# Kernel tuning notes

Measured on AMD Instinct MI355X. Metric: run time of the kernel, lower is better.

The kernel has to match this reference:

```python
import jax, jax.numpy as jnp
import numpy as np
import math

N, IN, H = 50000, 64, 128      # nodes, input feat, hidden dim
SH, HD = 8, 16                 # structural heads, dim per head (SH*HD == H)
TH, THD = 4, 32                # temporal heads, head dim
T, E, C = 8, 400000, 10        # snapshots, edges per snapshot, classes


def _ln(x, g, b):
    mu = jnp.mean(x, -1, keepdims=True)
    var = jnp.mean((x - mu) ** 2, -1, keepdims=True)
    return (x - mu) * jax.lax.rsqrt(var + 1e-5) * g + b


def _gat(x, ei, Wg, a, g, b):
    # x: [N,H], ei: [2,E]. Multi-head GAT with scatter softmax over dst.
    n = x.shape[0]
    h = (x @ Wg.T).reshape(n, SH, HD)
    src, dst = ei[0], ei[1]
    hs = h[src]                                  # [E,SH,HD] gathered src feats
    hd_ = h[dst]                                 # [E,SH,HD]
    s = jnp.concatenate([hs, hd_], -1) @ a       # [E,SH] shared attn vector per head
    s = jnp.where(s > 0, s, 0.2 * s)             # LeakyReLU(0.2)
    m = jax.ops.segment_max(s, dst, num_segments=n)   # [N,SH]
    e = jnp.exp(s - m[dst])
    z = jax.ops.segment_sum(e, dst, num_segments=n)   # [N,SH]
    alpha = e / z[dst]                           # scatter softmax per dst node
    msg = hs * alpha[..., None]                  # [E,SH,HD]
    out = jax.ops.segment_sum(msg.reshape(-1, SH * HD), dst, num_segments=n)
    out = out + x                                # residual (Identity: in_dim == SH*HD)
    return jax.nn.elu(_ln(out, g, b))


def setup_inputs():
    key = jax.random.key(0)
    ks = jax.random.split(key, 10)
    def xu(k, shape):
        lim = math.sqrt(6.0 / (shape[0] + shape[-1]))
        return jax.random.uniform(k, shape, minval=-lim, maxval=lim, dtype=jnp.float32)
    return {
        'x_original': jax.random.normal(ks[0], (N, IN), dtype=jnp.float32),
        'edge_indices': jax.random.randint(ks[1], (T, 2, E), 0, N),
        'node_masks': jnp.ones((T, N), dtype=jnp.int32),
        'Wp': xu(ks[2], (H, IN)), 'bp': jnp.zeros(H),
        'Wg': xu(ks[3], (H, H)),
        'a_attn': xu(ks[4], (1, 2 * HD))[0],
        'ln1_g': jnp.ones(H), 'ln1_b': jnp.zeros(H),
        'Wqkv': xu(ks[5], (3 * H, H)), 'bqkv': jnp.zeros(3 * H),
        'Wo': xu(ks[6], (H, H)), 'bo': jnp.zeros(H),
        'ln2_g': jnp.ones(H), 'ln2_b': jnp.zeros(H),
        'Wc': xu(ks[7], (C, H)), 'bc': jnp.zeros(C),
    }


def reference(x_original, edge_indices, node_masks, Wp, bp, Wg, a_attn, ln1_g, ln1_b,
              Wqkv, bqkv, Wo, bo, ln2_g, ln2_b, Wc, bc):
    # input projection (dropout is identity in eval)
    x = jax.nn.elu(x_original @ Wp.T + bp)                      # [N,H]
    # structural attention per snapshot (scan keeps one snapshot's edge buffers live)
    def step(_, ei):
        return None, _gat(x, ei, Wg, a_attn, ln1_g, ln1_b)
    _, seq = jax.lax.scan(step, None, edge_indices)             # [T,N,H]
    # sinusoidal positional encoding over time
    pos = jnp.arange(T, dtype=jnp.float32)[:, None]
    div = jnp.exp(jnp.arange(0, H, 2, dtype=jnp.float32) * (-math.log(10000.0) / H))
    pe = jnp.stack([jnp.sin(pos * div), jnp.cos(pos * div)], -1).reshape(T, H)
    seq_pe = seq + pe[:, None, :]
    # temporal self-attention over T per node
    qkv = (seq_pe @ Wqkv.T + bqkv).reshape(T, N, TH, 3 * THD).transpose(1, 2, 0, 3)
    q, k, v = jnp.split(qkv, 3, axis=-1)                        # each [N,TH,T,THD]
    attn = jax.nn.softmax(jnp.einsum('nhtd,nhsd->nhts', q, k) / math.sqrt(THD), -1)
    o = jnp.einsum('nhts,nhsd->nhtd', attn, v).transpose(2, 0, 1, 3).reshape(T, N, H)
    o = o @ Wo.T + bo
    out = jax.nn.elu(_ln(seq_pe + o, ln2_g, ln2_b))             # [T,N,H]
    final = out[-1]                                             # last time step
    return final @ Wc.T + bc                                    # [N,C] logits
```

## Files before the change

### kernel.cpp

```cpp
#include <hip/hip_runtime.h>
#include <hip/hip_bf16.h>
#include <math.h>

#define NN   50000
#define INF_ 64
#define HH   128
#define NSH  8
#define TT   8
#define EE   400000
#define CC   10

typedef __attribute__((ext_vector_type(8))) short short8;
typedef __attribute__((ext_vector_type(4))) short short4v;
typedef __attribute__((ext_vector_type(4))) float f32x4;

__device__ __forceinline__ float b2f(unsigned short u){
    unsigned v = ((unsigned)u) << 16; float f; __builtin_memcpy(&f, &v, 4); return f;
}
__device__ __forceinline__ unsigned short f2b(float f){
    unsigned x; __builtin_memcpy(&x, &f, 4);
    x += 0x7fffu + ((x >> 16) & 1u);
    return (unsigned short)(x >> 16);
}

__global__ __launch_bounds__(256) void k_wcvt(const float* __restrict__ Wqkv,
    const float* __restrict__ Wo, const float* __restrict__ Wp,
    const float* __restrict__ Wg, unsigned short* __restrict__ wkv,
    unsigned short* __restrict__ wq, unsigned short* __restrict__ wo_,
    unsigned short* __restrict__ wp_, unsigned short* __restrict__ wg_)
{
    int idx = blockIdx.x * 256 + threadIdx.x;
    if (idx < 32768) {
        int r = idx >> 7, c = idx & 127;
        int hh = r >> 6, rem = r & 63;
        wkv[idx] = f2b(Wqkv[(hh * 96 + 32 + rem) * HH + c]);
    } else if (idx < 49152) {
        int i2 = idx - 32768;
        int r = i2 >> 7, c = i2 & 127;
        int hh = r >> 5, dd = r & 31;
        wq[i2] = f2b(Wqkv[(hh * 96 + dd) * HH + c]);
    } else if (idx < 65536) {
        int i2 = idx - 49152;
        wo_[i2] = f2b(Wo[i2]);
    } else if (idx < 73728) {
        int i2 = idx - 65536;
        wp_[i2] = f2b(Wp[i2]);
    } else {
        int i2 = idx - 73728;
        wg_[i2] = f2b(Wg[i2]);
    }
}

__global__ __launch_bounds__(256) void k_projh(const float* __restrict__ xo,
    const unsigned short* __restrict__ wp, const float* __restrict__ bp,
    const unsigned short* __restrict__ wg, const float* __restrict__ a,
    unsigned short* __restrict__ xb, unsigned short* __restrict__ h,
    float* __restrict__ p1, float* __restrict__ p2)
{
    __shared__ __align__(16) char lds[40960];
    int tid = threadIdx.x;
    int n0 = blockIdx.x * 64;
    int wid = tid >> 6, lane = tid & 63, lm = lane & 15, kg = lane >> 4;

    for (int w = tid; w < 512; w += 256) {
        int row = w >> 3, u = w & 7;
        int nr = n0 + row; if (nr >= NN) nr = NN - 1;
        const float4* src = (const float4*)(xo + (size_t)nr * INF_ + u * 8);
        float4 v0 = src[0], v1 = src[1];
        short8 p;
        p[0] = (short)f2b(v0.x); p[1] = (short)f2b(v0.y);
        p[2] = (short)f2b(v0.z); p[3] = (short)f2b(v0.w);
        p[4] = (short)f2b(v1.x); p[5] = (short)f2b(v1.y);
        p[6] = (short)f2b(v1.z); p[7] = (short)f2b(v1.w);
        *(short8*)(lds + ((row * 128 + u * 16) ^ ((row & 7) << 4))) = p;
    }
    __syncthreads();

    short8 bf1[2][2];
    #pragma unroll
    for (int ntl = 0; ntl < 2; ++ntl)
        #pragma unroll
        for (int ks = 0; ks < 2; ++ks)
            bf1[ntl][ks] = *(const short8*)(wp + (size_t)(wid * 32 + ntl * 16 + lm) * INF_ + ks * 32 + kg * 8);
    f32x4 acc1[4][2];
    #pragma unroll
    for (int mt = 0; mt < 4; ++mt)
        #pragma unroll
        for (int ntl = 0; ntl < 2; ++ntl)
            acc1[mt][ntl] = (f32x4){0.f, 0.f, 0.f, 0.f};
    #pragma unroll
    for (int mt = 0; mt < 4; ++mt) {
        int row = mt * 16 + lm, swz = (row & 7) << 4, ab = row * 128;
        short8 af[2];
        #pragma unroll
        for (int ks = 0; ks < 2; ++ks)
            af[ks] = *(short8*)(lds + ((ab + ks * 64 + kg * 16) ^ swz));
        #pragma unroll
        for (int ntl = 0; ntl < 2; ++ntl)
            #pragma unroll
            for (int ks = 0; ks < 2; ++ks)
                acc1[mt][ntl] = __builtin_amdgcn_mfma_f32_16x16x32_bf16(
                    af[ks], bf1[ntl][ks], acc1[mt][ntl], 0, 0, 0);
    }

    #pragma unroll
    for (int mt = 0; mt < 4; ++mt)
        #pragma unroll
        for (int ntl = 0; ntl < 2; ++ntl) {
            int j = wid * 32 + ntl * 16 + lm;
            float bpj = bp[j];
            #pragma unroll
            for (int r = 0; r < 4; ++r) {
                int rowl = mt * 16 + kg * 4 + r;
                float v = acc1[mt][ntl][r] + bpj;
                v = v > 0.f ? v : (__expf(v) - 1.f);
                int node = n0 + rowl;
                unsigned short vb = f2b(v);
                if (node < NN) xb[(size_t)node * HH + j] = vb;
                *(unsigned short*)(lds + 8192 + ((rowl * 256 + j * 2) ^ ((rowl & 7) << 4))) = vb;
            }
        }
    __syncthreads();

    short8 bf2[2][4];
    #pragma unroll
    for (int ntl = 0; ntl < 2; ++ntl)
        #pragma unroll
        for (int ks = 0; ks < 4; ++ks)
            bf2[ntl][ks] = *(const short8*)(wg + (size_t)(wid * 32 + ntl * 16 + lm) * HH + ks * 32 + kg * 8);
    f32x4 acc2[4][2];
    #pragma unroll
    for (int mt = 0; mt < 4; ++mt)
        #pragma unroll
        for (int ntl = 0; ntl < 2; ++ntl)
            acc2[mt][ntl] = (f32x4){0.f, 0.f, 0.f, 0.f};
    #pragma unroll
    for (int mt = 0; mt < 4; ++mt) {
        int row = mt * 16 + lm, swz = (row & 7) << 4, ab = row * 256;
        short8 af[4];
        #pragma unroll
        for (int ks = 0; ks < 4; ++ks)
            af[ks] = *(short8*)(lds + 8192 + ((ab + ks * 64 + kg * 16) ^ swz));
        #pragma unroll
        for (int ntl = 0; ntl < 2; ++ntl)
            #pragma unroll
            for (int ks = 0; ks < 4; ++ks)
                acc2[mt][ntl] = __builtin_amdgcn_mfma_f32_16x16x32_bf16(
                    af[ks], bf2[ntl][ks], acc2[mt][ntl], 0, 0, 0);
    }

    float a1v = a[lm], a2v = a[16 + lm];
    #pragma unroll
    for (int mt = 0; mt < 4; ++mt)
        #pragma unroll
        for (int ntl = 0; ntl < 2; ++ntl) {
            int head = wid * 2 + ntl;
            int j = wid * 32 + ntl * 16 + lm;
            float c1r[4], c2r[4];
            #pragma unroll
            for (int r = 0; r < 4; ++r) {
                float hv = acc2[mt][ntl][r];
                int node = n0 + mt * 16 + kg * 4 + r;
                if (node < NN) h[(size_t)node * HH + j] = f2b(hv);
                c1r[r] = hv * a1v;
                c2r[r] = hv * a2v;
            }
            #pragma unroll
            for (int off = 1; off < 16; off <<= 1)
                #pragma unroll
                for (int r = 0; r < 4; ++r) {
                    c1r[r] += __shfl_xor(c1r[r], off);
                    c2r[r] += __shfl_xor(c2r[r], off);
                }
            if (lm == 0) {
                #pragma unroll
                for (int r = 0; r < 4; ++r) {
                    int node = n0 + mt * 16 + kg * 4 + r;
                    if (node < NN) {
                        p1[(size_t)node * NSH + head] = c1r[r];
                        p2[(size_t)node * NSH + head] = c2r[r];
                    }
                }
            }
        }
}

__global__ __launch_bounds__(256) void k_deg(const int* __restrict__ ei, int* __restrict__ deg)
{
    int e = blockIdx.x * 256 + threadIdx.x;
    int t = blockIdx.y;
    if (e >= EE) return;
    int dst = ei[(size_t)t * 2 * EE + EE + e];
    atomicAdd(&deg[t * NN + dst], 1);
}

#define NCH 49

__global__ __launch_bounds__(256) void k_scan1(const int* __restrict__ deg,
    int* __restrict__ csum)
{
    int t = blockIdx.y, c = blockIdx.x, tid = threadIdx.x;
    int base = c * 1024;
    int s = 0;
    #pragma unroll
    for (int k = 0; k < 4; ++k) {
        int i = base + k * 256 + tid;
        if (i < NN) s += deg[t * NN + i];
    }
    #pragma unroll
    for (int off = 32; off; off >>= 1) s += __shfl_xor(s, off);
    __shared__ int sm[4];
    if ((tid & 63) == 0) sm[tid >> 6] = s;
    __syncthreads();
    if (tid == 0) csum[t * NCH + c] = sm[0] + sm[1] + sm[2] + sm[3];
}

__global__ __launch_bounds__(64) void k_scan2(int* __restrict__ csum)
{
    int t = threadIdx.x;
    if (t >= TT) return;
    int run = 0;
    for (int c = 0; c < NCH; ++c) {
        int v = csum[t * NCH + c];
        csum[t * NCH + c] = run;
        run += v;
    }
}

__global__ __launch_bounds__(256) void k_scan3(const int* __restrict__ deg,
    const int* __restrict__ csum, int* __restrict__ rowptr, int* __restrict__ cur)
{
    int t = blockIdx.y, c = blockIdx.x, tid = threadIdx.x;
    int i0 = c * 1024 + tid * 4;
    int d[4];
    int s = 0;
    #pragma unroll
    for (int k = 0; k < 4; ++k) {
        d[k] = (i0 + k < NN) ? deg[t * NN + i0 + k] : 0;
        s += d[k];
    }
    __shared__ int sm[256];
    sm[tid] = s;
    __syncthreads();
    for (int off = 1; off < 256; off <<= 1) {
        int v = (tid >= off) ? sm[tid - off] : 0;
        __syncthreads();
        sm[tid] += v;
        __syncthreads();
    }
    int run = csum[t * NCH + c] + sm[tid] - s;
    #pragma unroll
    for (int k = 0; k < 4; ++k) {
        int i = i0 + k;
        if (i < NN) {
            rowptr[t * NN + i] = run;
            cur[t * NN + i] = run;
            run += d[k];
        }
    }
}

__global__ __launch_bounds__(256) void k_scatter(const int* __restrict__ ei,
    int* __restrict__ cur, int* __restrict__ esrc8)
{
    int e = blockIdx.x * 256 + threadIdx.x;
    int t = blockIdx.y;
    if (e >= EE) return;
    const int* eit = ei + (size_t)t * 2 * EE;
    int src = eit[e], dst = eit[EE + e];
    int pos = atomicAdd(&cur[t * NN + dst], 1);
    esrc8[(size_t)t * EE + pos] = src;
}

__global__ __launch_bounds__(256) void k_gat_node(const int* __restrict__ rowptr,
    const int* __restrict__ deg, const int* __restrict__ esrc8,
    const float* __restrict__ p1, const float* __restrict__ p2,
    const unsigned* __restrict__ h32, const unsigned* __restrict__ x32,
    const float* __restrict__ g, const float* __restrict__ b,
    unsigned* __restrict__ seq32)
{
    int lane = threadIdx.x & 63;
    int n = blockIdx.x * 4 + (threadIdx.x >> 6);
    int j0 = lane * 2;
    int head = lane >> 3;
    float p2h = p2[(size_t)n * NSH + head];
    unsigned xv = x32[(size_t)n * 64 + lane];
    float xv0 = b2f((unsigned short)xv), xv1 = b2f((unsigned short)(xv >> 16));
    float gj0 = g[j0], gj1 = g[j0 + 1], bj0 = b[j0], bj1 = b[j0 + 1];
    float dv = __expf((float)j0 * (-9.210340371976184f / 128.f));

    for (int t = 0; t < TT; ++t) {
        const int* es = esrc8 + (size_t)t * EE;
        int start = rowptr[t * NN + n], dg = deg[t * NN + n];

        float z = 0.f, a0 = 0.f, a1 = 0.f;
        if (dg <= 64) {
            int si = (lane < dg) ? es[start + lane] : 0x7fffffff;
            int cnt = 0;
            for (int jj = 0; jj < dg; ++jj) {
                int sj = __shfl(si, jj);
                cnt += (sj < si) || (sj == si && jj < lane);
            }
            int r = (lane < dg) ? cnt : lane;
            int sorted = __builtin_amdgcn_ds_permute(r << 2, si);

            int ee = 0;
            for (; ee + 1 < dg; ee += 2) {
                int s0 = __shfl(sorted, ee), s1 = __shfl(sorted, ee + 1);
                float v0 = p1[(size_t)s0 * NSH + head] + p2h;
                float v1 = p1[(size_t)s1 * NSH + head] + p2h;
                v0 = fmaxf(v0, 0.2f * v0);
                v1 = fmaxf(v1, 0.2f * v1);
                float e0 = __expf(v0), e1 = __expf(v1);
                unsigned hv0 = h32[(size_t)s0 * 64 + lane];
                unsigned hv1 = h32[(size_t)s1 * 64 + lane];
                z += e0 + e1;
                a0 = fmaf(e0, b2f((unsigned short)hv0), a0);
                a1 = fmaf(e0, b2f((unsigned short)(hv0 >> 16)), a1);
                a0 = fmaf(e1, b2f((unsigned short)hv1), a0);
                a1 = fmaf(e1, b2f((unsigned short)(hv1 >> 16)), a1);
            }
            if (ee < dg) {
                int s0 = __shfl(sorted, ee);
                float v0 = p1[(size_t)s0 * NSH + head] + p2h;
                v0 = fmaxf(v0, 0.2f * v0);
                float e0 = __expf(v0);
                unsigned hv0 = h32[(size_t)s0 * 64 + lane];
                z += e0;
                a0 = fmaf(e0, b2f((unsigned short)hv0), a0);
                a1 = fmaf(e0, b2f((unsigned short)(hv0 >> 16)), a1);
            }
        } else {
            for (int ee = 0; ee < dg; ++ee) {
                int s0 = es[start + ee];
                float v0 = p1[(size_t)s0 * NSH + head] + p2h;
                v0 = fmaxf(v0, 0.2f * v0);
                float e0 = __expf(v0);
                unsigned hv0 = h32[(size_t)s0 * 64 + lane];
                z += e0;
                a0 = fmaf(e0, b2f((unsigned short)hv0), a0);
                a1 = fmaf(e0, b2f((unsigned short)(hv0 >> 16)), a1);
            }
        }
        float rz = dg > 0 ? 1.f / z : 0.f;

        float v0 = a0 * rz + xv0, v1 = a1 * rz + xv1;
        float s1v = v0 + v1, s2v = v0 * v0 + v1 * v1;
        #pragma unroll
        for (int off = 32; off; off >>= 1) {
            s1v += __shfl_xor(s1v, off);
            s2v += __shfl_xor(s2v, off);
        }
        float mu  = s1v * (1.f / HH);
        float var = s2v * (1.f / HH) - mu * mu;
        float rstd = rsqrtf(var + 1e-5f);
        float y0 = (v0 - mu) * rstd * gj0 + bj0;
        float y1 = (v1 - mu) * rstd * gj1 + bj1;
        y0 = y0 > 0.f ? y0 : (__expf(y0) - 1.f);
        y1 = y1 > 0.f ? y1 : (__expf(y1) - 1.f);
        float ang = (float)t * dv;
        y0 += sinf(ang);
        y1 += cosf(ang);
        seq32[((size_t)t * NN + n) * 64 + lane] =
            (unsigned)f2b(y0) | ((unsigned)f2b(y1) << 16);
    }
}

#define Q_OFF 65536
#define O_OFF 69760
#define LDS_SZ 74112

__global__ __launch_bounds__(256, 2) void k_temporal(
    const unsigned short* __restrict__ seq, const unsigned short* __restrict__ wkv,
    const unsigned short* __restrict__ wq, const unsigned short* __restrict__ wo,
    const float* __restrict__ bqkv, const float* __restrict__ bo,
    const float* __restrict__ g2, const float* __restrict__ b2,
    const float* __restrict__ Wc, const float* __restrict__ bc,
    float* __restrict__ out)
{
    __shared__ __align__(16) char lds[LDS_SZ];
    unsigned short* Q_s = (unsigned short*)(lds + Q_OFF);
    unsigned short* o_s = (unsigned short*)(lds + O_OFF);
    float*          y_s = (float*)lds;

    int tid = threadIdx.x;
    int n0 = blockIdx.x * 16;
    int wid = tid >> 6, lane = tid & 63, lm = lane & 15, kg = lane >> 4;

    for (int w = tid; w < 2048; w += 256) {
        int r = w >> 4, u = w & 15;
        int t = r & 7, ln = r >> 3;
        int byte = (r * 256 + u * 16) ^ ((r & 7) << 4);
        *(short8*)(lds + byte) = *(const short8*)(seq + ((size_t)t * NN + n0 + ln) * HH + u * 8);
    }
    __syncthreads();

    short8 bf[4][4];
    #pragma unroll
    for (int ntl = 0; ntl < 4; ++ntl) {
        int T = wid * 4 + ntl;
        #pragma unroll
        for (int ks = 0; ks < 4; ++ks)
            bf[ntl][ks] = *(const short8*)(wkv + (size_t)(T * 16 + lm) * HH + ks * 32 + kg * 8);
    }
    f32x4 acc[8][4];
    #pragma unroll
    for (int mt = 0; mt < 8; ++mt)
        #pragma unroll
        for (int ntl = 0; ntl < 4; ++ntl)
            acc[mt][ntl] = (f32x4){0.f, 0.f, 0.f, 0.f};
    #pragma unroll
    for (int mt = 0; mt < 8; ++mt) {
        int arow = mt * 16 + lm;
        int ab = arow * 256, swz = (arow & 7) << 4;
        short8 af[4];
        #pragma unroll
        for (int ks = 0; ks < 4; ++ks)
            af[ks] = *(short8*)(lds + ((ab + ks * 64 + kg * 16) ^ swz));
        #pragma unroll
        for (int ntl = 0; ntl < 4; ++ntl)
            #pragma unroll
            for (int ks = 0; ks < 4; ++ks)
                acc[mt][ntl] = __builtin_amdgcn_mfma_f32_16x16x32_bf16(
                    af[ks], bf[ntl][ks], acc[mt][ntl], 0, 0, 0);
    }
    f32x4 qacc[2];
    qacc[0] = (f32x4){0.f,0.f,0.f,0.f}; qacc[1] = (f32x4){0.f,0.f,0.f,0.f};
    {
        int arow = lm * 8 + 7;
        int ab = arow * 256, swz = 7 << 4;
        short8 afq[4];
        #pragma unroll
        for (int ks = 0; ks < 4; ++ks)
            afq[ks] = *(short8*)(lds + ((ab + ks * 64 + kg * 16) ^ swz));
        #pragma unroll
        for (int q2 = 0; q2 < 2; ++q2) {
            int Tq = wid * 2 + q2;
            #pragma unroll
            for (int ks = 0; ks < 4; ++ks)
                qacc[q2] = __builtin_amdgcn_mfma_f32_16x16x32_bf16(
                    afq[ks], *(const short8*)(wq + (size_t)(Tq * 16 + lm) * HH + ks * 32 + kg * 8),
                    qacc[q2], 0, 0, 0);
        }
    }
    __syncthreads();

    #pragma unroll
    for (int mt = 0; mt < 8; ++mt)
        #pragma unroll
        for (int ntl = 0; ntl < 4; ++ntl) {
            int kvidx = (wid * 4 + ntl) * 16 + lm;
            int r0 = mt * 16 + kg * 4;
            int byte = (kvidx * 256 + r0 * 2) ^ ((kvidx & 7) << 4);
            unsigned p01 = (unsigned)f2b(acc[mt][ntl][0]) | ((unsigned)f2b(acc[mt][ntl][1]) << 16);
            unsigned p23 = (unsigned)f2b(acc[mt][ntl][2]) | ((unsigned)f2b(acc[mt][ntl][3]) << 16);
            *(unsigned*)(lds + byte)     = p01;
            *(unsigned*)(lds + byte + 4) = p23;
        }
    #pragma unroll
    for (int q2 = 0; q2 < 2; ++q2) {
        int qcol = (wid * 2 + q2) * 16 + lm;
        #pragma unroll
        for (int rg = 0; rg < 4; ++rg)
            Q_s[(kg * 4 + rg) * 132 + qcol] = f2b(qacc[q2][rg]);
    }
    __syncthreads();

    int sub = tid >> 7, j = tid & 127, hh = j >> 5, d = j & 31;
    float bq = bqkv[hh * 96 + d], bk = bqkv[hh * 96 + 32 + d], bv = bqkv[hh * 96 + 64 + d];
    int kidx = hh * 64 + d, vidx = hh * 64 + 32 + d;
    int kswz = (kidx & 7) << 4, vswz = (vidx & 7) << 4;
    #pragma unroll
    for (int it = 0; it < 8; ++it) {
        int ln = it * 2 + sub;
        int kb = (kidx * 256 + ln * 16) ^ kswz;
        int vb = (vidx * 256 + ln * 16) ^ vswz;
        short4v k01 = *(short4v*)(lds + kb);
        short4v k23 = *(short4v*)(lds + kb + 8);
        short4v v01 = *(short4v*)(lds + vb);
        short4v v23 = *(short4v*)(lds + vb + 8);
        float qv = b2f(Q_s[ln * 132 + j]) + bq;
        float kk[8] = {b2f((unsigned short)k01[0]), b2f((unsigned short)k01[1]),
                       b2f((unsigned short)k01[2]), b2f((unsigned short)k01[3]),
                       b2f((unsigned short)k23[0]), b2f((unsigned short)k23[1]),
                       b2f((unsigned short)k23[2]), b2f((unsigned short)k23[3])};
        float vvv[8] = {b2f((unsigned short)v01[0]), b2f((unsigned short)v01[1]),
                        b2f((unsigned short)v01[2]), b2f((unsigned short)v01[3]),
                        b2f((unsigned short)v23[0]), b2f((unsigned short)v23[1]),
                        b2f((unsigned short)v23[2]), b2f((unsigned short)v23[3])};
        float sc[8];
        #pragma unroll
        for (int t = 0; t < 8; ++t) {
            float p = qv * (kk[t] + bk);
            #pragma unroll
            for (int off = 16; off; off >>= 1) p += __shfl_xor(p, off);
            sc[t] = p * 0.17677669529663689f;
        }
        float mx = sc[0];
        #pragma unroll
        for (int t = 1; t < 8; ++t) mx = fmaxf(mx, sc[t]);
        float se = 0.f;
        #pragma unroll
        for (int t = 0; t < 8; ++t) { sc[t] = __expf(sc[t] - mx); se += sc[t]; }
        float inv = 1.f / se, ov = 0.f;
        #pragma unroll
        for (int t = 0; t < 8; ++t) ov = fmaf(sc[t] * inv, vvv[t] + bv, ov);
        o_s[ln * 136 + j] = f2b(ov);
    }
    __syncthreads();

    short8 af2[4];
    #pragma unroll
    for (int ks = 0; ks < 4; ++ks)
        af2[ks] = *(short8*)((char*)o_s + lm * 272 + ks * 64 + kg * 16);
    f32x4 yac[2];
    yac[0] = (f32x4){0.f,0.f,0.f,0.f}; yac[1] = (f32x4){0.f,0.f,0.f,0.f};
    #pragma unroll
    for (int q2 = 0; q2 < 2; ++q2) {
        int col0 = (wid * 2 + q2) * 16;
        #pragma unroll
        for (int ks = 0; ks < 4; ++ks)
            yac[q2] = __builtin_amdgcn_mfma_f32_16x16x32_bf16(
                af2[ks], *(const short8*)(wo + (size_t)(col0 + lm) * HH + ks * 32 + kg * 8),
                yac[q2], 0, 0, 0);
    }
    #pragma unroll
    for (int q2 = 0; q2 < 2; ++q2) {
        int col0 = (wid * 2 + q2) * 16;
        #pragma unroll
        for (int rg = 0; rg < 4; ++rg)
            y_s[(kg * 4 + rg) * 132 + col0 + lm] = yac[q2][rg];
    }
    __syncthreads();

    #pragma unroll
    for (int it2 = 0; it2 < 4; ++it2) {
        int row = it2 * 4 + wid;
        int j0 = 2 * lane;
        float2 yv  = *(float2*)(y_s + row * 132 + j0);
        float2 bov = *(const float2*)(bo + j0);
        unsigned s7 = *(const unsigned*)(seq + ((size_t)7 * NN + n0 + row) * HH + j0);
        float y0 = yv.x + bov.x + b2f((unsigned short)s7);
        float y1 = yv.y + bov.y + b2f((unsigned short)(s7 >> 16));
        float s1 = y0 + y1, s2 = y0 * y0 + y1 * y1;
        #pragma unroll
        for (int off = 32; off; off >>= 1) { s1 += __shfl_xor(s1, off); s2 += __shfl_xor(s2, off); }
        float mu  = s1 * (1.f / HH);
        float var = s2 * (1.f / HH) - mu * mu;
        float rstd = rsqrtf(var + 1e-5f);
        float2 gv  = *(const float2*)(g2 + j0);
        float2 bvv = *(const float2*)(b2 + j0);
        float f0 = (y0 - mu) * rstd * gv.x + bvv.x;
        float f1 = (y1 - mu) * rstd * gv.y + bvv.y;
        f0 = f0 > 0.f ? f0 : (__expf(f0) - 1.f);
        f1 = f1 > 0.f ? f1 : (__expf(f1) - 1.f);
        y_s[row * 132 + j0]     = f0;
        y_s[row * 132 + j0 + 1] = f1;
    }
    __syncthreads();

    if (tid < 160) {
        int ln = tid / 10, c = tid - ln * 10;
        float a = bc[c];
        const float* wc = Wc + c * HH;
        #pragma unroll 8
        for (int i = 0; i < HH; ++i) a = fmaf(wc[i], y_s[ln * 132 + i], a);
        out[(size_t)(n0 + ln) * CC + c] = a;
    }
}

extern "C" void kernel_launch(void* const* d_in, const int* in_sizes, int n_in,
                              void* d_out, int out_size, void* d_ws, size_t ws_size,
                              hipStream_t stream)
{
    const float* xo   = (const float*)d_in[0];
    const int*   ei   = (const int*)d_in[1];
    const float* Wp   = (const float*)d_in[3];
    const float* bp   = (const float*)d_in[4];
    const float* Wg   = (const float*)d_in[5];
    const float* a    = (const float*)d_in[6];
    const float* g1   = (const float*)d_in[7];
    const float* b1   = (const float*)d_in[8];
    const float* Wqkv = (const float*)d_in[9];
    const float* bqkv = (const float*)d_in[10];
    const float* Wo   = (const float*)d_in[11];
    const float* bo   = (const float*)d_in[12];
    const float* g2   = (const float*)d_in[13];
    const float* b2   = (const float*)d_in[14];
    const float* Wc   = (const float*)d_in[15];
    const float* bc   = (const float*)d_in[16];
    float* out = (float*)d_out;

    char* W = (char*)d_ws;
    unsigned short* xb     = (unsigned short*)(W + 0);
    float*          p1     = (float*)(W + 12800000);
    float*          p2     = (float*)(W + 14400000);
    unsigned short* h      = (unsigned short*)(W + 16000000);
    unsigned short* seq    = (unsigned short*)(W + 28800000);
    int*            deg    = (int*)(W + 131200000);
    int*            rowptr = (int*)(W + 132800000);
    int*            cur    = (int*)(W + 134400000);
    int*            esrc8  = (int*)(W + 136000000);
    unsigned short* wkv    = (unsigned short*)(W + 148800000);
    unsigned short* wq     = (unsigned short*)(W + 148865536);
    unsigned short* wo     = (unsigned short*)(W + 148898304);
    unsigned short* wp_b   = (unsigned short*)(W + 148931072);
    unsigned short* wg_b   = (unsigned short*)(W + 148947456);
    int*            csum   = (int*)(W + 148980224);
    if (ws_size < (size_t)148981808) return;

    hipMemsetAsync(deg, 0, (size_t)TT * NN * sizeof(int), stream);

    k_wcvt   <<<352, 256, 0, stream>>>(Wqkv, Wo, Wp, Wg, wkv, wq, wo, wp_b, wg_b);
    k_projh  <<<(NN + 63) / 64, 256, 0, stream>>>(xo, wp_b, bp, wg_b, a, xb, h, p1, p2);
    k_deg    <<<dim3((EE + 255) / 256, TT), 256, 0, stream>>>(ei, deg);
    k_scan1  <<<dim3(NCH, TT), 256, 0, stream>>>(deg, csum);
    k_scan2  <<<1, 64, 0, stream>>>(csum);
    k_scan3  <<<dim3(NCH, TT), 256, 0, stream>>>(deg, csum, rowptr, cur);
    k_scatter<<<dim3((EE + 255) / 256, TT), 256, 0, stream>>>(ei, cur, esrc8);
    k_gat_node<<<NN / 4, 256, 0, stream>>>(rowptr, deg, esrc8, p1, p2,
                                           (const unsigned*)h, (const unsigned*)xb,
                                           g1, b1, (unsigned*)seq);
    k_temporal<<<NN / 16, 256, 0, stream>>>(seq, wkv, wq, wo, bqkv, bo,
                                            g2, b2, Wc, bc, out);
}
```

Before: 759.0 us.

## Fold deg memset into weight convert, use exp2, 32-bit indexing, wider LDS swizzle

Zeroes the degree array inside the weight-conversion kernel instead of a separate memset launch, and bounds the last conversion branch. It pre-scales the attention vector by log2(e) so the GAT node kernel can use exp2f instead of __expf. It switches the GAT gather indices to 32-bit unsigned arithmetic to cut 64-bit address math, and widens the temporal kernel's LDS XOR swizzle from 8 to 16 rows to reduce bank conflicts. The main risks are 32-bit index overflow, which the current sizes appear to stay within, and swizzle consistency across all LDS accesses.

Measured after the change: 764.4 us, median of 2. No clear change (+0.7%).

```diff
diff --git a/kernel.cpp b/kernel.cpp
--- a/kernel.cpp
+++ b/kernel.cpp
@@ -27,9 +27,11 @@
     const float* __restrict__ Wo, const float* __restrict__ Wp,
     const float* __restrict__ Wg, unsigned short* __restrict__ wkv,
     unsigned short* __restrict__ wq, unsigned short* __restrict__ wo_,
-    unsigned short* __restrict__ wp_, unsigned short* __restrict__ wg_)
+    unsigned short* __restrict__ wp_, unsigned short* __restrict__ wg_,
+    int* __restrict__ deg)
 {
     int idx = blockIdx.x * 256 + threadIdx.x;
+    for (int i = idx; i < TT * NN; i += 352 * 256) deg[i] = 0;
     if (idx < 32768) {
         int r = idx >> 7, c = idx & 127;
         int hh = r >> 6, rem = r & 63;
@@ -45,7 +47,7 @@
     } else if (idx < 73728) {
         int i2 = idx - 65536;
         wp_[i2] = f2b(Wp[i2]);
-    } else {
+    } else if (idx < 90112) {
         int i2 = idx - 73728;
         wg_[i2] = f2b(Wg[i2]);
     }
@@ -149,7 +151,7 @@
                     af[ks], bf2[ntl][ks], acc2[mt][ntl], 0, 0, 0);
     }
 
-    float a1v = a[lm], a2v = a[16 + lm];
+    float a1v = a[lm] * 1.44269504088896f, a2v = a[16 + lm] * 1.44269504088896f;
     #pragma unroll
     for (int mt = 0; mt < 4; ++mt)
         #pragma unroll
@@ -283,8 +285,8 @@
     int n = blockIdx.x * 4 + (threadIdx.x >> 6);
     int j0 = lane * 2;
     int head = lane >> 3;
-    float p2h = p2[(size_t)n * NSH + head];
-    unsigned xv = x32[(size_t)n * 64 + lane];
+    float p2h = p2[(unsigned)(n * NSH + head)];
+    unsigned xv = x32[(unsigned)(n * 64 + lane)];
     float xv0 = b2f((unsigned short)xv), xv1 = b2f((unsigned short)(xv >> 16));
     float gj0 = g[j0], gj1 = g[j0 + 1], bj0 = b[j0], bj1 = b[j0 + 1];
     float dv = __expf((float)j0 * (-9.210340371976184f / 128.f));
@@ -295,7 +297,7 @@
 
         float z = 0.f, a0 = 0.f, a1 = 0.f;
         if (dg <= 64) {
-            int si = (lane < dg) ? es[start + lane] : 0x7fffffff;
+            int si = (lane < dg) ? es[(unsigned)(start + lane)] : 0x7fffffff;
             int cnt = 0;
             for (int jj = 0; jj < dg; ++jj) {
                 int sj = __shfl(si, jj);
@@ -307,13 +309,13 @@
             int ee = 0;
             for (; ee + 1 < dg; ee += 2) {
                 int s0 = __shfl(sorted, ee), s1 = __shfl(sorted, ee + 1);
-                float v0 = p1[(size_t)s0 * NSH + head] + p2h;
-                float v1 = p1[(size_t)s1 * NSH + head] + p2h;
+                float v0 = p1[(unsigned)(s0 * NSH + head)] + p2h;
+                float v1 = p1[(unsigned)(s1 * NSH + head)] + p2h;
                 v0 = fmaxf(v0, 0.2f * v0);
                 v1 = fmaxf(v1, 0.2f * v1);
-                float e0 = __expf(v0), e1 = __expf(v1);
-                unsigned hv0 = h32[(size_t)s0 * 64 + lane];
-                unsigned hv1 = h32[(size_t)s1 * 64 + lane];
+                float e0 = exp2f(v0), e1 = exp2f(v1);
+                unsigned hv0 = h32[(unsigned)(s0 * 64 + lane)];
+                unsigned hv1 = h32[(unsigned)(s1 * 64 + lane)];
                 z += e0 + e1;
                 a0 = fmaf(e0, b2f((unsigned short)hv0), a0);
                 a1 = fmaf(e0, b2f((unsigned short)(hv0 >> 16)), a1);
@@ -322,21 +324,21 @@
             }
             if (ee < dg) {
                 int s0 = __shfl(sorted, ee);
-                float v0 = p1[(size_t)s0 * NSH + head] + p2h;
+                float v0 = p1[(unsigned)(s0 * NSH + head)] + p2h;
                 v0 = fmaxf(v0, 0.2f * v0);
-                float e0 = __expf(v0);
-                unsigned hv0 = h32[(size_t)s0 * 64 + lane];
+                float e0 = exp2f(v0);
+                unsigned hv0 = h32[(unsigned)(s0 * 64 + lane)];
                 z += e0;
                 a0 = fmaf(e0, b2f((unsigned short)hv0), a0);
                 a1 = fmaf(e0, b2f((unsigned short)(hv0 >> 16)), a1);
             }
         } else {
             for (int ee = 0; ee < dg; ++ee) {
-                int s0 = es[start + ee];
-                float v0 = p1[(size_t)s0 * NSH + head] + p2h;
+                int s0 = es[(unsigned)(start + ee)];
+                float v0 = p1[(unsigned)(s0 * NSH + head)] + p2h;
                 v0 = fmaxf(v0, 0.2f * v0);
-                float e0 = __expf(v0);
-                unsigned hv0 = h32[(size_t)s0 * 64 + lane];
+                float e0 = exp2f(v0);
+                unsigned hv0 = h32[(unsigned)(s0 * 64 + lane)];
                 z += e0;
                 a0 = fmaf(e0, b2f((unsigned short)hv0), a0);
                 a1 = fmaf(e0, b2f((unsigned short)(hv0 >> 16)), a1);
@@ -361,7 +363,7 @@
         float ang = (float)t * dv;
         y0 += sinf(ang);
         y1 += cosf(ang);
-        seq32[((size_t)t * NN + n) * 64 + lane] =
+        seq32[(unsigned)((t * NN + n) * 64 + lane)] =
             (unsigned)f2b(y0) | ((unsigned)f2b(y1) << 16);
     }
 }
@@ -390,7 +392,7 @@
     for (int w = tid; w < 2048; w += 256) {
         int r = w >> 4, u = w & 15;
         int t = r & 7, ln = r >> 3;
-        int byte = (r * 256 + u * 16) ^ ((r & 7) << 4);
+        int byte = (r * 256 + u * 16) ^ ((r & 15) << 4);
         *(short8*)(lds + byte) = *(const short8*)(seq + ((size_t)t * NN + n0 + ln) * HH + u * 8);
     }
     __syncthreads();
@@ -412,7 +414,7 @@
     #pragma unroll
     for (int mt = 0; mt < 8; ++mt) {
         int arow = mt * 16 + lm;
-        int ab = arow * 256, swz = (arow & 7) << 4;
+        int ab = arow * 256, swz = (arow & 15) << 4;
         short8 af[4];
         #pragma unroll
         for (int ks = 0; ks < 4; ++ks)
@@ -428,7 +430,7 @@
     qacc[0] = (f32x4){0.f,0.f,0.f,0.f}; qacc[1] = (f32x4){0.f,0.f,0.f,0.f};
     {
         int arow = lm * 8 + 7;
-        int ab = arow * 256, swz = 7 << 4;
+        int ab = arow * 256, swz = (arow & 15) << 4;
         short8 afq[4];
         #pragma unroll
         for (int ks = 0; ks < 4; ++ks)
@@ -451,7 +453,7 @@
         for (int ntl = 0; ntl < 4; ++ntl) {
             int kvidx = (wid * 4 + ntl) * 16 + lm;
             int r0 = mt * 16 + kg * 4;
-            int byte = (kvidx * 256 + r0 * 2) ^ ((kvidx & 7) << 4);
+            int byte = (kvidx * 256 + r0 * 2) ^ ((kvidx & 15) << 4);
             unsigned p01 = (unsigned)f2b(acc[mt][ntl][0]) | ((unsigned)f2b(acc[mt][ntl][1]) << 16);
             unsigned p23 = (unsigned)f2b(acc[mt][ntl][2]) | ((unsigned)f2b(acc[mt][ntl][3]) << 16);
             *(unsigned*)(lds + byte)     = p01;
@@ -469,7 +471,7 @@
     int sub = tid >> 7, j = tid & 127, hh = j >> 5, d = j & 31;
     float bq = bqkv[hh * 96 + d], bk = bqkv[hh * 96 + 32 + d], bv = bqkv[hh * 96 + 64 + d];
     int kidx = hh * 64 + d, vidx = hh * 64 + 32 + d;
-    int kswz = (kidx & 7) << 4, vswz = (vidx & 7) << 4;
+    int kswz = (kidx & 15) << 4, vswz = (vidx & 15) << 4;
     #pragma unroll
     for (int it = 0; it < 8; ++it) {
         int ln = it * 2 + sub;
@@ -609,9 +611,7 @@
     int*            csum   = (int*)(W + 148980224);
     if (ws_size < (size_t)148981808) return;
 
-    hipMemsetAsync(deg, 0, (size_t)TT * NN * sizeof(int), stream);
-
-    k_wcvt   <<<352, 256, 0, stream>>>(Wqkv, Wo, Wp, Wg, wkv, wq, wo, wp_b, wg_b);
+    k_wcvt   <<<352, 256, 0, stream>>>(Wqkv, Wo, Wp, Wg, wkv, wq, wo, wp_b, wg_b, deg);
     k_projh  <<<(NN + 63) / 64, 256, 0, stream>>>(xo, wp_b, bp, wg_b, a, xb, h, p1, p2);
     k_deg    <<<dim3((EE + 255) / 256, TT), 256, 0, stream>>>(ei, deg);
     k_scan1  <<<dim3(NCH, TT), 256, 0, stream>>>(deg, csum);
```
